# Kernel tuning notes

Measured on AMD Instinct MI355X. Metric: run time of the kernel, lower is better.

## Reference

```python
import jax, jax.numpy as jnp
import numpy as np

D_MODEL = 1024
N_HEADS = 16
HEAD_DIM = D_MODEL // N_HEADS


def setup_inputs() -> dict:
    key = jax.random.key(0)
    ks = jax.random.split(key, 5)
    s = 0.02  # small init scale to keep softmax numerics reasonable
    x = jax.random.normal(ks[0], (4, 2048, D_MODEL), dtype=jnp.float32)
    w_qkv = jax.random.normal(ks[1], (D_MODEL, 3 * D_MODEL), dtype=jnp.float32) * s
    b_qkv = jnp.zeros((3 * D_MODEL,), dtype=jnp.float32)
    w_proj = jax.random.normal(ks[2], (D_MODEL, D_MODEL), dtype=jnp.float32) * s
    b_proj = jnp.zeros((D_MODEL,), dtype=jnp.float32)
    return {"x": x, "w_qkv": w_qkv, "b_qkv": b_qkv, "w_proj": w_proj, "b_proj": b_proj}


def reference(x, w_qkv, b_qkv, w_proj, b_proj):
    B, T, C = x.shape
    scale = 1.0 / np.sqrt(HEAD_DIM)
    qkv = x @ w_qkv + b_qkv                               # [B,T,3C]
    qkv = qkv.reshape(B, T, 3, N_HEADS, HEAD_DIM)
    q = qkv[:, :, 0].transpose(0, 2, 1, 3)               # [B,H,T,D]
    k = qkv[:, :, 1].transpose(0, 2, 1, 3)
    v = qkv[:, :, 2].transpose(0, 2, 1, 3)
    att = jnp.einsum('bhqd,bhkd->bhqk', q, k) * scale    # [B,H,T,T]
    causal = jnp.tril(jnp.ones((T, T), dtype=bool))
    att = jnp.where(causal, att, -jnp.inf)
    att = jax.nn.softmax(att, axis=-1)
    y = jnp.einsum('bhqk,bhkd->bhqd', att, v)            # [B,H,T,D]
    y = y.transpose(0, 2, 1, 3).reshape(B, T, C)
    y = y @ w_proj + b_proj
    return y
```

## Files before the change

kernel.cpp:

```cpp
#include <hip/hip_runtime.h>
#include <stdint.h>

#define BATCH 4
#define SEQ 2048
#define DMODEL 1024
#define NHEADS 16
#define HDIM 64
#define MROWS (BATCH * SEQ)

typedef float floatx4 __attribute__((ext_vector_type(4)));
typedef __bf16 bf16x8 __attribute__((ext_vector_type(8)));
typedef __bf16 bf16x4 __attribute__((ext_vector_type(4)));
typedef short short8 __attribute__((ext_vector_type(8)));

__device__ __forceinline__ unsigned short f32_to_bf16(float f) {
    union { float f; unsigned int u; } c; c.f = f;
    unsigned int u = c.u;
    unsigned int r = (u + 0x7FFFu + ((u >> 16) & 1u)) >> 16;
    return (unsigned short)r;
}

__device__ __forceinline__ void async_ld16(const void* g, void* l) {
    __builtin_amdgcn_global_load_lds(
        (const __attribute__((address_space(1))) unsigned int*)g,
        (__attribute__((address_space(3))) unsigned int*)l, 16, 0, 0);
}

__global__ __launch_bounds__(256) void prep_kernel(
    const float* __restrict__ x, unsigned short* __restrict__ xb,
    const float* __restrict__ w_qkv, unsigned short* __restrict__ wqkvT,
    const float* __restrict__ w_proj, unsigned short* __restrict__ wprojT) {
    const int gx = blockIdx.x, gy = blockIdx.y;
    const int tx = threadIdx.x, ty = threadIdx.y;
    if (gx < 256) {
        int i = (gx * 32 + gy) * 256 + ty * 32 + tx;
        float4 v = ((const float4*)x)[i];
        ushort4 o;
        o.x = f32_to_bf16(v.x); o.y = f32_to_bf16(v.y);
        o.z = f32_to_bf16(v.z); o.w = f32_to_bf16(v.w);
        ((ushort4*)xb)[i] = o;
        return;
    }
    __shared__ float tile[32][33];
    const float* in; unsigned short* out; int N, bx;
    if (gx < 352) { in = w_qkv; out = wqkvT; N = 3072; bx = (gx - 256) * 32; }
    else          { in = w_proj; out = wprojT; N = 1024; bx = (gx - 352) * 32; }
    const int by = gy * 32;
#pragma unroll
    for (int i = 0; i < 4; ++i)
        tile[ty + i * 8][tx] = in[(size_t)(by + ty + i * 8) * N + bx + tx];
    __syncthreads();
#pragma unroll
    for (int i = 0; i < 4; ++i)
        out[(size_t)(bx + ty + i * 8) * DMODEL + by + tx] = f32_to_bf16(tile[tx][ty + i * 8]);
}

__global__ __launch_bounds__(256) void transp_bf16_head(
    const unsigned short* __restrict__ in, unsigned short* __restrict__ out) {
    __shared__ unsigned short tile[32][33];
    const unsigned short* src = in + (size_t)blockIdx.z * SEQ * HDIM;
    unsigned short* dst = out + (size_t)blockIdx.z * SEQ * HDIM;
    int bx = blockIdx.x * 32;
    int by = blockIdx.y * 32;
    int tx = threadIdx.x, ty = threadIdx.y;
#pragma unroll
    for (int i = 0; i < 4; ++i)
        tile[ty + i * 8][tx] = src[(size_t)(by + ty + i * 8) * HDIM + bx + tx];
    __syncthreads();
#pragma unroll
    for (int i = 0; i < 4; ++i) {
        int keyg = by + tx;
        int col2 = (keyg & ~63) | (((keyg & 15) << 2) | ((keyg >> 4) & 3));
        dst[(size_t)(bx + ty + i * 8) * SEQ + col2] = tile[tx][ty + i * 8];
    }
}

template <int EPI>
__global__ __launch_bounds__(256, 3) void gemm_bt(
    const unsigned short* __restrict__ A, const unsigned short* __restrict__ Bt,
    const float* __restrict__ bias, float* __restrict__ Cout,
    unsigned short* __restrict__ Qo, unsigned short* __restrict__ Ko,
    unsigned short* __restrict__ Vo, int M, int N, int K) {
    __shared__ __align__(16) unsigned short As[3][128 * 32];
    __shared__ __align__(16) unsigned short Bs[3][128 * 32];
    const int tid = threadIdx.x;
    const int lane = tid & 63;
    const int w = tid >> 6;
    const int wm = w & 1, wn = w >> 1;
    const int quad = lane >> 4, l16 = lane & 15;

    const int nbx = gridDim.x;
    const int nwg = nbx * gridDim.y;
    const int lin = blockIdx.y * nbx + blockIdx.x;
    const int swz = (lin & 7) * (nwg >> 3) + (lin >> 3);
    const int m0 = (swz / nbx) * 128;
    const int n0 = (swz % nbx) * 128;
    const int fsw = (l16 >> 1) & 3;

    const int idx0 = tid, idx1 = tid + 256;
    const int row0 = idx0 >> 2, row1 = idx1 >> 2;
    const int cg0 = (idx0 & 3) ^ ((row0 >> 1) & 3);
    const int cg1 = (idx1 & 3) ^ ((row1 >> 1) & 3);
    const unsigned short* Ar0 = &A[(size_t)(m0 + row0) * K + cg0 * 8];
    const unsigned short* Ar1 = &A[(size_t)(m0 + row1) * K + cg1 * 8];
    const unsigned short* Br0 = &Bt[(size_t)(n0 + row0) * K + cg0 * 8];
    const unsigned short* Br1 = &Bt[(size_t)(n0 + row1) * K + cg1 * 8];

    floatx4 acc[4][4];
#pragma unroll
    for (int mt = 0; mt < 4; ++mt)
#pragma unroll
        for (int nt = 0; nt < 4; ++nt) acc[mt][nt] = (floatx4){0.f, 0.f, 0.f, 0.f};

    async_ld16(Ar0, &As[0][idx0 * 8]);
    async_ld16(Br0, &Bs[0][idx0 * 8]);
    async_ld16(Ar1, &As[0][idx1 * 8]);
    async_ld16(Br1, &Bs[0][idx1 * 8]);
    async_ld16(Ar0 + 32, &As[1][idx0 * 8]);
    async_ld16(Br0 + 32, &Bs[1][idx0 * 8]);
    async_ld16(Ar1 + 32, &As[1][idx1 * 8]);
    async_ld16(Br1 + 32, &Bs[1][idx1 * 8]);

    const int nk = K >> 5;
    int bcur = 0, bpre = 2;
    for (int kt = 0; kt < nk; ++kt) {
        if (kt + 2 < nk)
            asm volatile("s_waitcnt vmcnt(4)" ::: "memory");
        else
            asm volatile("s_waitcnt vmcnt(0)" ::: "memory");
        __builtin_amdgcn_s_barrier();
        asm volatile("" ::: "memory");

        if (kt + 2 < nk) {
            const int ko = (kt + 2) << 5;
            async_ld16(Ar0 + ko, &As[bpre][idx0 * 8]);
            async_ld16(Br0 + ko, &Bs[bpre][idx0 * 8]);
            async_ld16(Ar1 + ko, &As[bpre][idx1 * 8]);
            async_ld16(Br1 + ko, &Bs[bpre][idx1 * 8]);
        }

        bf16x8 aF[4], bF[4];
#pragma unroll
        for (int mt = 0; mt < 4; ++mt)
            aF[mt] = *(const bf16x8*)&As[bcur][(wm * 64 + mt * 16 + l16) * 32 + (quad ^ fsw) * 8];
#pragma unroll
        for (int nt = 0; nt < 4; ++nt)
            bF[nt] = *(const bf16x8*)&Bs[bcur][(wn * 64 + nt * 16 + l16) * 32 + (quad ^ fsw) * 8];
#pragma unroll
        for (int mt = 0; mt < 4; ++mt)
#pragma unroll
            for (int nt = 0; nt < 4; ++nt)
                acc[mt][nt] = __builtin_amdgcn_mfma_f32_16x16x32_bf16(
                    aF[mt], bF[nt], acc[mt][nt], 0, 0, 0);

        bcur = (bcur == 2) ? 0 : bcur + 1;
        bpre = (bpre == 2) ? 0 : bpre + 1;
    }

#pragma unroll
    for (int mt = 0; mt < 4; ++mt)
#pragma unroll
        for (int nt = 0; nt < 4; ++nt)
#pragma unroll
            for (int r = 0; r < 4; ++r) {
                int m = m0 + wm * 64 + mt * 16 + quad * 4 + r;
                int n = n0 + wn * 64 + nt * 16 + l16;
                float v = acc[mt][nt][r] + bias[n];
                if (EPI == 1) {
                    Cout[(size_t)m * N + n] = v;
                } else {
                    int sel = n >> 10, c = n & 1023;
                    int head = c >> 6, d = c & 63;
                    int bb = m >> 11, t = m & 2047;
                    unsigned short* dst = sel == 0 ? Qo : (sel == 1 ? Ko : Vo);
                    dst[((((size_t)bb * NHEADS + head) * SEQ + t) << 6) + d] = f32_to_bf16(v);
                }
            }
}

__device__ __forceinline__ void strip_body(
    int kb, int rowb, int quad, int l16,
    const bf16x8 (&qf)[2][2], const unsigned short* Kb, const unsigned short* Vb,
    unsigned short* Pw, bf16x8 ones, float csc,
    floatx4 (&o)[2][4], floatx4 (&lsum)[2]) {
    floatx4 s[2][4];
#pragma unroll
    for (int mt = 0; mt < 2; ++mt)
#pragma unroll
        for (int nt = 0; nt < 4; ++nt) s[mt][nt] = (floatx4){0.f, 0.f, 0.f, 0.f};
#pragma unroll
    for (int kk = 0; kk < 2; ++kk) {
        bf16x8 kf[4];
#pragma unroll
        for (int nt = 0; nt < 4; ++nt)
            kf[nt] = *(const bf16x8*)&Kb[(nt * 16 + l16) * 64 +
                                         ((kk * 4 + quad) ^ (l16 & 7)) * 8];
#pragma unroll
        for (int nt = 0; nt < 4; ++nt)
#pragma unroll
            for (int mt = 0; mt < 2; ++mt)
                s[mt][nt] = __builtin_amdgcn_mfma_f32_16x16x32_bf16(
                    qf[mt][kk], kf[nt], s[mt][nt], 0, 0, 0);
    }

    if ((kb * 64 + 63) > rowb) {
#pragma unroll
        for (int mt = 0; mt < 2; ++mt)
#pragma unroll
            for (int nt = 0; nt < 4; ++nt)
#pragma unroll
                for (int r = 0; r < 4; ++r) {
                    int key = kb * 64 + nt * 16 + l16;
                    int qrow = rowb + mt * 16 + quad * 4 + r;
                    if (key > qrow) s[mt][nt][r] = -INFINITY;
                }
    }

#pragma unroll
    for (int mt = 0; mt < 2; ++mt)
#pragma unroll
        for (int nt = 0; nt < 4; ++nt)
#pragma unroll
            for (int r = 0; r < 4; ++r)
                s[mt][nt][r] = __builtin_amdgcn_exp2f(s[mt][nt][r] * csc);

#pragma unroll
    for (int mt = 0; mt < 2; ++mt)
#pragma unroll
        for (int r = 0; r < 4; ++r) {
            int prow = mt * 16 + quad * 4 + r;
            int unit = l16 ^ (prow & 14);
            floatx4 t = {s[mt][0][r], s[mt][1][r], s[mt][2][r], s[mt][3][r]};
            bf16x4 pv = __builtin_convertvector(t, bf16x4);
            *(bf16x4*)&Pw[prow * 64 + unit * 4] = pv;
        }

#pragma unroll
    for (int kk = 0; kk < 2; ++kk) {
        bf16x8 af[2];
#pragma unroll
        for (int mt = 0; mt < 2; ++mt) {
            int prow = mt * 16 + l16;
            int u2 = (kk * 8 + quad * 2) ^ (l16 & 14);
            af[mt] = *(const bf16x8*)&Pw[prow * 64 + u2 * 4];
        }
#pragma unroll
        for (int nt = 0; nt < 4; ++nt) {
            bf16x8 vf = *(const bf16x8*)&Vb[(nt * 16 + l16) * 64 +
                                            ((kk * 4 + quad) ^ (l16 & 7)) * 8];
#pragma unroll
            for (int mt = 0; mt < 2; ++mt)
                o[mt][nt] = __builtin_amdgcn_mfma_f32_16x16x32_bf16(
                    af[mt], vf, o[mt][nt], 0, 0, 0);
        }
#pragma unroll
        for (int mt = 0; mt < 2; ++mt)
            lsum[mt] = __builtin_amdgcn_mfma_f32_16x16x32_bf16(
                af[mt], ones, lsum[mt], 0, 0, 0);
    }
}

__global__ __launch_bounds__(256, 2) void attn_kernel(
    const unsigned short* __restrict__ Qg, const unsigned short* __restrict__ Kg,
    const unsigned short* __restrict__ Vtg, unsigned short* __restrict__ Yatt) {
    __shared__ __align__(16) unsigned short Kb2[3][4096];
    __shared__ __align__(16) unsigned short Vb2[3][4096];
    __shared__ __align__(16) unsigned short Ps[4][2048];

    const int tid = threadIdx.x;
    const int lane = tid & 63;
    const int w = tid >> 6;
    const int quad = lane >> 4, l16 = lane & 15;
    const int bh = blockIdx.x;
    const int by = blockIdx.y;
    const int sA = by * 4 + w;
    const size_t base = (size_t)bh * SEQ * HDIM;
    const int bIdx = bh >> 4, h = bh & 15;
    unsigned short* Pw = &Ps[w][0];
    const float csc = 0.18033688f;

    const int lrow = lane >> 3;
    const int lch = (lane & 7) ^ lrow;

    short8 osv = {0x3F80, 0x3F80, 0x3F80, 0x3F80, 0x3F80, 0x3F80, 0x3F80, 0x3F80};
    bf16x8 ones = __builtin_bit_cast(bf16x8, osv);

    const int rowbA = sA * 32;
    const int rowbB = (63 - sA) * 32;
    const int tA = 2 * by + 2, tB = 32 - 2 * by;
    const int kmaxB = tA > tB ? tA : tB;
    const int lastA = sA >> 1;
    const int lastB = (2047 - 32 * sA) >> 6;

    const unsigned short* Ktg = Kg + base;
    const unsigned short* Vtg_t = Vtg + base;
    const int i0 = w * 2, i1 = w * 2 + 1;
    const int kof0 = (i0 * 8 + lrow) * 64 + lch * 8;
    const int kof1 = (i1 * 8 + lrow) * 64 + lch * 8;
    const size_t vof0 = (size_t)(i0 * 8 + lrow) * SEQ + lch * 8;
    const size_t vof1 = (size_t)(i1 * 8 + lrow) * SEQ + lch * 8;
    const int ld0 = i0 * 512 + lane * 8;
    const int ld1 = i1 * 512 + lane * 8;

    bf16x8 qfA[2][2], qfB[2][2];
#pragma unroll
    for (int mt = 0; mt < 2; ++mt)
#pragma unroll
        for (int kk = 0; kk < 2; ++kk) {
            qfA[mt][kk] = *(const bf16x8*)&Qg[base + (size_t)(rowbA + mt * 16 + l16) * 64 +
                                              kk * 32 + quad * 8];
            qfB[mt][kk] = *(const bf16x8*)&Qg[base + (size_t)(rowbB + mt * 16 + l16) * 64 +
                                              kk * 32 + quad * 8];
        }
    asm volatile("" ::: "memory");

    floatx4 lsumA[2], lsumB[2];
    floatx4 oA[2][4], oB[2][4];
#pragma unroll
    for (int mt = 0; mt < 2; ++mt) {
        lsumA[mt] = (floatx4){0.f, 0.f, 0.f, 0.f};
        lsumB[mt] = (floatx4){0.f, 0.f, 0.f, 0.f};
#pragma unroll
        for (int nt = 0; nt < 4; ++nt) {
            oA[mt][nt] = (floatx4){0.f, 0.f, 0.f, 0.f};
            oB[mt][nt] = (floatx4){0.f, 0.f, 0.f, 0.f};
        }
    }

    async_ld16(Ktg + kof0, &Kb2[0][ld0]);
    async_ld16(Vtg_t + vof0, &Vb2[0][ld0]);
    async_ld16(Ktg + kof1, &Kb2[0][ld1]);
    async_ld16(Vtg_t + vof1, &Vb2[0][ld1]);
    async_ld16(Ktg + 64 * HDIM + kof0, &Kb2[1][ld0]);
    async_ld16(Vtg_t + 64 + vof0, &Vb2[1][ld0]);
    async_ld16(Ktg + 64 * HDIM + kof1, &Kb2[1][ld1]);
    async_ld16(Vtg_t + 64 + vof1, &Vb2[1][ld1]);

    int bcur = 0, bpre = 2;
    for (int kb = 0; kb < kmaxB; ++kb) {
        if (kb + 2 < kmaxB)
            asm volatile("s_waitcnt vmcnt(4)" ::: "memory");
        else
            asm volatile("s_waitcnt vmcnt(0)" ::: "memory");
        __builtin_amdgcn_s_barrier();
        asm volatile("" ::: "memory");

        if (kb + 2 < kmaxB) {
            const unsigned short* Kt2 = Ktg + (size_t)(kb + 2) * 64 * HDIM;
            const unsigned short* Vt2 = Vtg_t + (kb + 2) * 64;
            async_ld16(Kt2 + kof0, &Kb2[bpre][ld0]);
            async_ld16(Vt2 + vof0, &Vb2[bpre][ld0]);
            async_ld16(Kt2 + kof1, &Kb2[bpre][ld1]);
            async_ld16(Vt2 + vof1, &Vb2[bpre][ld1]);
        }

        if (kb <= lastA)
            strip_body(kb, rowbA, quad, l16, qfA, &Kb2[bcur][0], &Vb2[bcur][0],
                       Pw, ones, csc, oA, lsumA);
        if (kb <= lastB)
            strip_body(kb, rowbB, quad, l16, qfB, &Kb2[bcur][0], &Vb2[bcur][0],
                       Pw, ones, csc, oB, lsumB);

        bcur = (bcur == 2) ? 0 : bcur + 1;
        bpre = (bpre == 2) ? 0 : bpre + 1;
    }

#pragma unroll
    for (int mt = 0; mt < 2; ++mt)
#pragma unroll
        for (int r = 0; r < 4; ++r) {
            float invA = 1.0f / lsumA[mt][r];
            float invB = 1.0f / lsumB[mt][r];
            int qrowA = rowbA + mt * 16 + quad * 4 + r;
            int qrowB = rowbB + mt * 16 + quad * 4 + r;
#pragma unroll
            for (int nt = 0; nt < 4; ++nt) {
                Yatt[((size_t)(bIdx * SEQ + qrowA) << 10) + h * 64 + nt * 16 + l16] =
                    f32_to_bf16(oA[mt][nt][r] * invA);
                Yatt[((size_t)(bIdx * SEQ + qrowB) << 10) + h * 64 + nt * 16 + l16] =
                    f32_to_bf16(oB[mt][nt][r] * invB);
            }
        }
}

extern "C" void kernel_launch(void* const* d_in, const int* in_sizes, int n_in,
                              void* d_out, int out_size, void* d_ws, size_t ws_size,
                              hipStream_t stream) {
    const float* x = (const float*)d_in[0];
    const float* w_qkv = (const float*)d_in[1];
    const float* b_qkv = (const float*)d_in[2];
    const float* w_proj = (const float*)d_in[3];
    const float* b_proj = (const float*)d_in[4];
    float* out = (float*)d_out;

    char* ws = (char*)d_ws;
    unsigned short* xb     = (unsigned short*)(ws);
    unsigned short* wqkvT  = (unsigned short*)(ws + 16777216);
    unsigned short* wprojT = (unsigned short*)(ws + 23068672);
    unsigned short* Qb     = (unsigned short*)(ws + 25165824);
    unsigned short* Kb     = (unsigned short*)(ws + 41943040);
    unsigned short* Vb     = (unsigned short*)(ws + 58720256);
    unsigned short* Yatt   = (unsigned short*)(ws + 75497472);
    unsigned short* Vt     = (unsigned short*)(ws + 92274688);

    prep_kernel<<<dim3(384, 32), dim3(32, 8), 0, stream>>>(x, xb, w_qkv, wqkvT,
                                                           w_proj, wprojT);
    gemm_bt<0><<<dim3(24, 64), 256, 0, stream>>>(xb, wqkvT, b_qkv, nullptr, Qb, Kb, Vb,
                                                 MROWS, 3 * DMODEL, DMODEL);
    transp_bf16_head<<<dim3(2, 64, BATCH * NHEADS), dim3(32, 8), 0, stream>>>(Vb, Vt);
    attn_kernel<<<dim3(64, 8), 256, 0, stream>>>(Qb, Kb, Vt, Yatt);
    gemm_bt<1><<<dim3(8, 64), 256, 0, stream>>>(Yatt, wprojT, b_proj, out, nullptr, nullptr,
                                                nullptr, MROWS, DMODEL, DMODEL);
}
```

Before: 248.8 us.

## Fuse V transpose into QKV GEMM epilogue via shared-memory staging

The QKV GEMM epilogue now handles V tiles itself. It stages them through a unified shared-memory buffer, applies the key-permuted transpose, and writes Vt directly. This removes the separate transp_bf16_head kernel launch and the round trip of V through global memory. The cost is extra LDS traffic and barriers in the V-producing blocks, plus a padded 132-stride staging layout that reuses the pipeline buffer.

```diff
diff --git a/kernel.cpp b/kernel.cpp
--- a/kernel.cpp
+++ b/kernel.cpp
@@ -55,34 +55,13 @@
         out[(size_t)(bx + ty + i * 8) * DMODEL + by + tx] = f32_to_bf16(tile[tx][ty + i * 8]);
 }
 
-__global__ __launch_bounds__(256) void transp_bf16_head(
-    const unsigned short* __restrict__ in, unsigned short* __restrict__ out) {
-    __shared__ unsigned short tile[32][33];
-    const unsigned short* src = in + (size_t)blockIdx.z * SEQ * HDIM;
-    unsigned short* dst = out + (size_t)blockIdx.z * SEQ * HDIM;
-    int bx = blockIdx.x * 32;
-    int by = blockIdx.y * 32;
-    int tx = threadIdx.x, ty = threadIdx.y;
-#pragma unroll
-    for (int i = 0; i < 4; ++i)
-        tile[ty + i * 8][tx] = src[(size_t)(by + ty + i * 8) * HDIM + bx + tx];
-    __syncthreads();
-#pragma unroll
-    for (int i = 0; i < 4; ++i) {
-        int keyg = by + tx;
-        int col2 = (keyg & ~63) | (((keyg & 15) << 2) | ((keyg >> 4) & 3));
-        dst[(size_t)(bx + ty + i * 8) * SEQ + col2] = tile[tx][ty + i * 8];
-    }
-}
-
 template <int EPI>
 __global__ __launch_bounds__(256, 3) void gemm_bt(
     const unsigned short* __restrict__ A, const unsigned short* __restrict__ Bt,
     const float* __restrict__ bias, float* __restrict__ Cout,
     unsigned short* __restrict__ Qo, unsigned short* __restrict__ Ko,
     unsigned short* __restrict__ Vo, int M, int N, int K) {
-    __shared__ __align__(16) unsigned short As[3][128 * 32];
-    __shared__ __align__(16) unsigned short Bs[3][128 * 32];
+    __shared__ __align__(16) unsigned short SM[24576];
     const int tid = threadIdx.x;
     const int lane = tid & 63;
     const int w = tid >> 6;
@@ -112,14 +91,14 @@
 #pragma unroll
         for (int nt = 0; nt < 4; ++nt) acc[mt][nt] = (floatx4){0.f, 0.f, 0.f, 0.f};
 
-    async_ld16(Ar0, &As[0][idx0 * 8]);
-    async_ld16(Br0, &Bs[0][idx0 * 8]);
-    async_ld16(Ar1, &As[0][idx1 * 8]);
-    async_ld16(Br1, &Bs[0][idx1 * 8]);
-    async_ld16(Ar0 + 32, &As[1][idx0 * 8]);
-    async_ld16(Br0 + 32, &Bs[1][idx0 * 8]);
-    async_ld16(Ar1 + 32, &As[1][idx1 * 8]);
-    async_ld16(Br1 + 32, &Bs[1][idx1 * 8]);
+    async_ld16(Ar0, &SM[idx0 * 8]);
+    async_ld16(Br0, &SM[12288 + idx0 * 8]);
+    async_ld16(Ar1, &SM[idx1 * 8]);
+    async_ld16(Br1, &SM[12288 + idx1 * 8]);
+    async_ld16(Ar0 + 32, &SM[4096 + idx0 * 8]);
+    async_ld16(Br0 + 32, &SM[16384 + idx0 * 8]);
+    async_ld16(Ar1 + 32, &SM[4096 + idx1 * 8]);
+    async_ld16(Br1 + 32, &SM[16384 + idx1 * 8]);
 
     const int nk = K >> 5;
     int bcur = 0, bpre = 2;
@@ -133,19 +112,21 @@
 
         if (kt + 2 < nk) {
             const int ko = (kt + 2) << 5;
-            async_ld16(Ar0 + ko, &As[bpre][idx0 * 8]);
-            async_ld16(Br0 + ko, &Bs[bpre][idx0 * 8]);
-            async_ld16(Ar1 + ko, &As[bpre][idx1 * 8]);
-            async_ld16(Br1 + ko, &Bs[bpre][idx1 * 8]);
+            async_ld16(Ar0 + ko, &SM[bpre * 4096 + idx0 * 8]);
+            async_ld16(Br0 + ko, &SM[12288 + bpre * 4096 + idx0 * 8]);
+            async_ld16(Ar1 + ko, &SM[bpre * 4096 + idx1 * 8]);
+            async_ld16(Br1 + ko, &SM[12288 + bpre * 4096 + idx1 * 8]);
         }
 
         bf16x8 aF[4], bF[4];
 #pragma unroll
         for (int mt = 0; mt < 4; ++mt)
-            aF[mt] = *(const bf16x8*)&As[bcur][(wm * 64 + mt * 16 + l16) * 32 + (quad ^ fsw) * 8];
+            aF[mt] = *(const bf16x8*)&SM[bcur * 4096 +
+                                         (wm * 64 + mt * 16 + l16) * 32 + (quad ^ fsw) * 8];
 #pragma unroll
         for (int nt = 0; nt < 4; ++nt)
-            bF[nt] = *(const bf16x8*)&Bs[bcur][(wn * 64 + nt * 16 + l16) * 32 + (quad ^ fsw) * 8];
+            bF[nt] = *(const bf16x8*)&SM[12288 + bcur * 4096 +
+                                         (wn * 64 + nt * 16 + l16) * 32 + (quad ^ fsw) * 8];
 #pragma unroll
         for (int mt = 0; mt < 4; ++mt)
 #pragma unroll
@@ -155,6 +136,34 @@
 
         bcur = (bcur == 2) ? 0 : bcur + 1;
         bpre = (bpre == 2) ? 0 : bpre + 1;
+    }
+
+    if (EPI == 0 && n0 >= 2048) {
+        const int hbase = (n0 - 2048) >> 6;
+        const int bb = m0 >> 11, t0 = m0 & 2047;
+        __syncthreads();
+#pragma unroll
+        for (int mt = 0; mt < 4; ++mt)
+#pragma unroll
+            for (int nt = 0; nt < 4; ++nt)
+#pragma unroll
+                for (int r = 0; r < 4; ++r) {
+                    int tl = wm * 64 + mt * 16 + quad * 4 + r;
+                    int nl = wn * 64 + nt * 16 + l16;
+                    int c2 = (tl & 64) | ((tl & 15) << 2) | ((tl >> 4) & 3);
+                    float v = acc[mt][nt][r] + bias[n0 + nl];
+                    SM[nl * 132 + c2] = f32_to_bf16(v);
+                }
+        __syncthreads();
+        const int rr = tid >> 1, hh = tid & 1;
+        const int head = hbase + (rr >> 6), d = rr & 63;
+        unsigned short* drow = Vo + ((size_t)(bb * NHEADS + head)) * SEQ * HDIM +
+                               (size_t)d * SEQ + t0 + hh * 64;
+        const unsigned short* srow = &SM[rr * 132 + hh * 64];
+#pragma unroll
+        for (int c = 0; c < 16; ++c)
+            *(bf16x4*)&drow[c * 4] = *(const bf16x4*)&srow[c * 4];
+        return;
     }
 
 #pragma unroll
@@ -172,7 +181,7 @@
                     int sel = n >> 10, c = n & 1023;
                     int head = c >> 6, d = c & 63;
                     int bb = m >> 11, t = m & 2047;
-                    unsigned short* dst = sel == 0 ? Qo : (sel == 1 ? Ko : Vo);
+                    unsigned short* dst = sel == 0 ? Qo : Ko;
                     dst[((((size_t)bb * NHEADS + head) * SEQ + t) << 6) + d] = f32_to_bf16(v);
                 }
             }
@@ -399,15 +408,13 @@
     unsigned short* wprojT = (unsigned short*)(ws + 23068672);
     unsigned short* Qb     = (unsigned short*)(ws + 25165824);
     unsigned short* Kb     = (unsigned short*)(ws + 41943040);
-    unsigned short* Vb     = (unsigned short*)(ws + 58720256);
     unsigned short* Yatt   = (unsigned short*)(ws + 75497472);
     unsigned short* Vt     = (unsigned short*)(ws + 92274688);
 
     prep_kernel<<<dim3(384, 32), dim3(32, 8), 0, stream>>>(x, xb, w_qkv, wqkvT,
                                                            w_proj, wprojT);
-    gemm_bt<0><<<dim3(24, 64), 256, 0, stream>>>(xb, wqkvT, b_qkv, nullptr, Qb, Kb, Vb,
+    gemm_bt<0><<<dim3(24, 64), 256, 0, stream>>>(xb, wqkvT, b_qkv, nullptr, Qb, Kb, Vt,
                                                  MROWS, 3 * DMODEL, DMODEL);
-    transp_bf16_head<<<dim3(2, 64, BATCH * NHEADS), dim3(32, 8), 0, stream>>>(Vb, Vt);
     attn_kernel<<<dim3(64, 8), 256, 0, stream>>>(Qb, Kb, Vt, Yatt);
     gemm_bt<1><<<dim3(8, 64), 256, 0, stream>>>(Yatt, wprojT, b_proj, out, nullptr, nullptr,
                                                 nullptr, MROWS, DMODEL, DMODEL);
```

New measurement: 237.0 us. -4.8%, faster.
